# Optimization experiments

Hardware: AMD Instinct MI355X
Metric: run time of the kernel (lower is better)

Reference implementation:

```python
import jax, jax.numpy as jnp
import numpy as np
import math

D_MODEL = 1024
N_HEADS = 16
D_FF = 4096
B, T = 2, 2048
EPS = 1e-5


def setup_inputs() -> dict:
    key = jax.random.key(0)
    ks = jax.random.split(key, 8)
    s = 0.02
    return {
        "x": jax.random.normal(ks[0], (B, T, D_MODEL), jnp.float32),
        "wq": jax.random.normal(ks[1], (D_MODEL, D_MODEL), jnp.float32) * s,
        "wk": jax.random.normal(ks[2], (D_MODEL, D_MODEL), jnp.float32) * s,
        "wv": jax.random.normal(ks[3], (D_MODEL, D_MODEL), jnp.float32) * s,
        "wo": jax.random.normal(ks[4], (D_MODEL, D_MODEL), jnp.float32) * s,
        "ln1_w": jnp.ones((D_MODEL,), jnp.float32),
        "ln2_w": jnp.ones((D_MODEL,), jnp.float32),
        "w1": jax.random.normal(ks[5], (D_FF, D_MODEL), jnp.float32) * s,
        "w2": jax.random.normal(ks[6], (D_MODEL, D_FF), jnp.float32) * s,
    }


def rmsnorm(x, w):
    # weight * x / sqrt(mean(x^2) + eps)
    denom = jnp.sqrt(jnp.mean(jnp.square(x), axis=-1, keepdims=True) + EPS)
    return w * x / denom


def mhsa(x, wq, wk, wv, wo):
    b, t, d = x.shape
    dk = d // N_HEADS
    # Linear(weight shape (out,in)): y = x @ W.T
    q = (x @ wq.T).reshape(b, t, N_HEADS, dk).transpose(0, 2, 1, 3)  # bhtd
    k = (x @ wk.T).reshape(b, t, N_HEADS, dk).transpose(0, 2, 1, 3)
    v = (x @ wv.T).reshape(b, t, N_HEADS, dk).transpose(0, 2, 1, 3)
    scores = jnp.einsum("bhqd,bhkd->bhqk", q, k) / math.sqrt(dk)
    causal = jnp.tril(jnp.ones((t, t), bool))  # True = keep
    scores = jnp.where(causal, scores, -jnp.inf)
    probs = jax.nn.softmax(scores, axis=-1)
    out = jnp.einsum("bhqk,bhkd->bhqd", probs, v)
    out = out.transpose(0, 2, 1, 3).reshape(b, t, d)
    return out @ wo.T


def ffn(x, w1, w2):
    h = jax.nn.gelu(x @ w1.T, approximate=False)  # exact erf GELU
    return h @ w2.T


def reference(x, wq, wk, wv, wo, ln1_w, ln2_w, w1, w2):
    x = x + mhsa(rmsnorm(x, ln1_w), wq, wk, wv, wo)
    x = x + ffn(rmsnorm(x, ln2_w), w1, w2)
    return x
```

## Files before the change

kernel.cpp:

```cpp
#include <hip/hip_runtime.h>
#include <stdint.h>

#define D_MODEL 1024
#define N_HEADS 16
#define D_FF    4096
#define BATCH   2
#define SEQ     2048
#define EPSV    1e-5f
#define MTOK    (BATCH*SEQ)
#define QKVS    3072


typedef __bf16 bf16x8 __attribute__((ext_vector_type(8)));
typedef float  f32x4  __attribute__((ext_vector_type(4)));

#define MFMA_BF16(a,b,c) __builtin_amdgcn_mfma_f32_16x16x32_bf16((a),(b),(c),0,0,0)

__device__ __forceinline__ float b2f(unsigned short u) {
  union { unsigned int i; float f; } c; c.i = ((unsigned int)u) << 16; return c.f;
}
__device__ __forceinline__ unsigned short f2b(float f) {
  union { float f; unsigned int i; } c; c.f = f;
  unsigned int x = c.i;
  unsigned int r = (x + 0x7fffu + ((x >> 16) & 1u)) >> 16;
  return (unsigned short)r;
}
__device__ __forceinline__ unsigned short f2b_trunc(float f) {
  union { float f; unsigned int i; } c; c.f = f;
  return (unsigned short)(c.i >> 16);
}

__device__ __forceinline__ void glds16(const unsigned short* g, unsigned short* l) {
  __builtin_amdgcn_global_load_lds(
      (const __attribute__((address_space(1))) void*)g,
      (__attribute__((address_space(3))) void*)l, 16, 0, 0);
}

__global__ void detect_kernel(const unsigned int* __restrict__ ln1, int* __restrict__ flag) {
  if (threadIdx.x == 0 && blockIdx.x == 0)
    *flag = (ln1[0] == 0x3F800000u) ? 1 : 0;
}

__global__ void convert_all_kernel(
    const void* __restrict__ wq, const void* __restrict__ wk,
    const void* __restrict__ wv, const void* __restrict__ wo,
    const void* __restrict__ w1, const void* __restrict__ w2,
    const void* __restrict__ l1, const void* __restrict__ l2,
    unsigned short* dq, unsigned short* dk, unsigned short* dv, unsigned short* dwo,
    unsigned short* d1, unsigned short* d2, unsigned short* dl1, unsigned short* dl2,
    const int* __restrict__ flag) {
  const int i = blockIdx.x * 256 + threadIdx.x;
  const void* src; unsigned short* dst; int off;
  if (i < 1048576) {
    const int t = i >> 18;  off = i & 262143;
    src = (t == 0) ? wq : (t == 1) ? wk : (t == 2) ? wv : wo;
    dst = (t == 0) ? dq : (t == 1) ? dk : (t == 2) ? dv : dwo;
  } else if (i < 2097152) { off = i - 1048576; src = w1; dst = d1; }
  else if (i < 3145728)   { off = i - 2097152; src = w2; dst = d2; }
  else if (i < 3145984)   { off = i - 3145728; src = l1; dst = dl1; }
  else                    { off = i - 3145984; src = l2; dst = dl2; }
  if (*flag) {
    const float4 v = ((const float4*)src)[off];
    ushort4 o; o.x = f2b(v.x); o.y = f2b(v.y); o.z = f2b(v.z); o.w = f2b(v.w);
    ((ushort4*)dst)[off] = o;
  } else {
    ((ushort4*)dst)[off] = ((const ushort4*)src)[off];
  }
}

__global__ void rmsnorm_kernel(const void* __restrict__ xin,
                               const unsigned short* __restrict__ w,
                               unsigned short* __restrict__ out,
                               const int* __restrict__ f32flag) {
  __shared__ float red[4];
  const int row = blockIdx.x;
  const int tid = threadIdx.x;
  const int base = tid * 4;
  const bool f32 = f32flag && (*f32flag != 0);
  float v0, v1, v2, v3;
  if (f32) {
    const float4 p = ((const float4*)xin)[(size_t)row * 256 + tid];
    v0 = p.x; v1 = p.y; v2 = p.z; v3 = p.w;
  } else {
    const short4 p = *(const short4*)((const unsigned short*)xin + (size_t)row * D_MODEL + base);
    v0 = b2f((unsigned short)p.x); v1 = b2f((unsigned short)p.y);
    v2 = b2f((unsigned short)p.z); v3 = b2f((unsigned short)p.w);
  }
  float ss = v0*v0 + v1*v1 + v2*v2 + v3*v3;
  #pragma unroll
  for (int d = 1; d < 64; d <<= 1) ss += __shfl_xor(ss, d);
  if ((tid & 63) == 0) red[tid >> 6] = ss;
  __syncthreads();
  const float tot = red[0] + red[1] + red[2] + red[3];
  const float inv = 1.0f / sqrtf(tot * (1.0f / (float)D_MODEL) + EPSV);
  short4 ov;
  ov.x = (short)f2b(b2f(w[base + 0]) * v0 * inv);
  ov.y = (short)f2b(b2f(w[base + 1]) * v1 * inv);
  ov.z = (short)f2b(b2f(w[base + 2]) * v2 * inv);
  ov.w = (short)f2b(b2f(w[base + 3]) * v3 * inv);
  *(short4*)(out + (size_t)row * D_MODEL + base) = ov;
}

#define BM 128
template<int TBN, int KSEG, int TBK>
__global__ __launch_bounds__(256 * KSEG) void gemm_bt_kernel(
    const unsigned short* __restrict__ A,
    const unsigned short* __restrict__ Bw,
    void* __restrict__ C,
    const void* __restrict__ R,
    int M, int N, int K, int flags,
    const int* __restrict__ outf32_flag,
    const int* __restrict__ resf32_flag) {
  constexpr int JN = TBN / 32;
  constexpr int SR = TBK / 8;
  constexpr int SH = (TBK == 32) ? 1 : 0;
  constexpr int SM = SR - 1;
  constexpr int GA = BM * SR;
  constexpr int GT = (BM + TBN) * SR;
  constexpr int KH = TBK / 32;
  __shared__ __align__(16) unsigned short smem[KSEG * (BM + TBN) * TBK];
  unsigned short* Asb = smem;
  unsigned short* Bsb = smem + KSEG * BM * TBK;

  const int tid   = threadIdx.x;
  const int tid_l = tid & 255;
  const int w     = tid >> 6;
  const int kseg  = (KSEG == 1) ? 0 : (w >> 2);
  const int wm    = (w >> 1) & 1, wn = w & 1;
  const int ln    = tid & 63;
  const int lm    = ln & 15, quad = ln >> 4;
  unsigned short* As = Asb + kseg * BM * TBK;
  unsigned short* Bs = Bsb + kseg * TBN * TBK;

  const int gx = gridDim.x;
  const int L  = blockIdx.x + gx * blockIdx.y;
  const int per = (gx * gridDim.y) >> 3;
  const int tile = (L & 7) * per + (L >> 3);
  const int tileM = (tile / gx) * BM;
  const int tileN = (tile % gx) * TBN;

  const int kofs = kseg * (K / KSEG);

  f32x4 acc[4][JN];
  #pragma unroll
  for (int i = 0; i < 4; i++)
    #pragma unroll
    for (int j = 0; j < JN; j++) acc[i][j] = (f32x4){0.f, 0.f, 0.f, 0.f};

  for (int k0 = 0; k0 < K / KSEG; k0 += TBK) {
    __syncthreads();
    #pragma unroll
    for (int g0 = 0; g0 < GT; g0 += 256) {
      const int g = g0 + tid_l;
      if (g0 + 256 <= GA || g < GA) {
        const int r  = g / SR;
        const int sg = (g & SM) ^ ((r >> SH) & SM);
        glds16(&A[(size_t)(tileM + r) * K + kofs + k0 + sg * 8], &As[g * 8]);
      } else {
        const int gb = g - GA;
        const int r  = gb / SR;
        const int sg = (gb & SM) ^ ((r >> SH) & SM);
        glds16(&Bw[(size_t)(tileN + r) * K + kofs + k0 + sg * 8], &Bs[gb * 8]);
      }
    }
    __syncthreads();

    #pragma unroll
    for (int hh = 0; hh < KH; hh++) {
      bf16x8 af[4], bfr[JN];
      #pragma unroll
      for (int i = 0; i < 4; i++) {
        const int r = wm * 64 + i * 16 + lm;
        const int p = (hh * 4 + quad) ^ ((r >> SH) & SM);
        af[i] = *(const bf16x8*)&As[r * TBK + p * 8];
      }
      #pragma unroll
      for (int j = 0; j < JN; j++) {
        const int r = wn * (TBN / 2) + j * 16 + lm;
        const int p = (hh * 4 + quad) ^ ((r >> SH) & SM);
        bfr[j] = *(const bf16x8*)&Bs[r * TBK + p * 8];
      }
      #pragma unroll
      for (int i = 0; i < 4; i++)
        #pragma unroll
        for (int j = 0; j < JN; j++)
          acc[i][j] = MFMA_BF16(af[i], bfr[j], acc[i][j]);
    }
  }

  if constexpr (KSEG == 2) {
    float* scratch = (float*)smem;
    #pragma unroll
    for (int j = 0; j < JN; j++) {
      __syncthreads();
      if (kseg == 1) {
        #pragma unroll
        for (int i = 0; i < 4; i++)
          #pragma unroll
          for (int r = 0; r < 4; r++)
            scratch[tid_l * 16 + i * 4 + r] = acc[i][j][r];
      }
      __syncthreads();
      if (kseg == 0) {
        #pragma unroll
        for (int i = 0; i < 4; i++)
          #pragma unroll
          for (int r = 0; r < 4; r++)
            acc[i][j][r] += scratch[tid_l * 16 + i * 4 + r];
      }
    }
  }

  if (kseg == 0) {
    const bool hasR   = flags & 2;
    const bool dogelu = flags & 8;
    const bool outf32 = outf32_flag && (*outf32_flag != 0);
    const bool rf32   = resf32_flag && (*resf32_flag != 0);
    #pragma unroll
    for (int i = 0; i < 4; i++) {
      #pragma unroll
      for (int j = 0; j < JN; j++) {
        #pragma unroll
        for (int r = 0; r < 4; r++) {
          const int row = tileM + wm * 64 + i * 16 + quad * 4 + r;
          const int col = tileN + wn * (TBN / 2) + j * 16 + lm;
          float val = acc[i][j][r];
          if (dogelu) {
            const float u = 0.7978845608f * (val + 0.044715f * val * val * val);
            const float e = exp2f(u * 2.885390082f);
            val = val - val * __builtin_amdgcn_rcpf(e + 1.0f);
          }
          const size_t idx = (size_t)row * N + col;
          if (hasR) val += rf32 ? ((const float*)R)[idx]
                                : b2f(((const unsigned short*)R)[idx]);
          if (outf32) ((float*)C)[idx] = val;
          else        ((unsigned short*)C)[idx] = f2b(val);
        }
      }
    }
  }
}

__global__ __launch_bounds__(256) void attn_kernel(
    const unsigned short* __restrict__ QKV,
    unsigned short* __restrict__ O) {
  __shared__ __align__(16) unsigned short Ks [2][64 * 64];
  __shared__ __align__(16) unsigned short VTs[2][64 * 64];
  __shared__ __align__(16) unsigned short Ps [4][16 * 64];

  const int tid = threadIdx.x;
  const int w = tid >> 6, ln = tid & 63;
  const int lm = ln & 15, quad = ln >> 4;
  const f32x4 zf = (f32x4){0.f, 0.f, 0.f, 0.f};

  const int L   = blockIdx.x;
  const int xcd = L & 7;
  const int idx = L >> 3;
  const int bh  = xcd * 4 + (idx >> 4);
  const int pr  = idx & 15;
  const int b   = bh >> 4, h = bh & 15;
  const int qtA = pr, qtB = 31 - pr;
  const int nA = qtA + 1, total = nA + qtB + 1;

  const unsigned short* Qp = QKV + (size_t)b * SEQ * QKVS + h * 64;
  const unsigned short* Kp = Qp + 1024;
  const unsigned short* Vp = Qp + 2048;

  auto scale8 = [](bf16x8 v) -> bf16x8 {
    union { bf16x8 h; unsigned short u[8]; } in, out;
    in.h = v;
    #pragma unroll
    for (int ii = 0; ii < 8; ii++) out.u[ii] = f2b(b2f(in.u[ii]) * 0.1803368801f);
    return out.h;
  };

  bf16x8 qfA0, qfA1, qfB0, qfB1;
  {
    const size_t ra = (size_t)(qtA * 64 + w * 16 + lm) * QKVS;
    qfA0 = scale8(*(const bf16x8*)&Qp[ra + quad * 8]);
    qfA1 = scale8(*(const bf16x8*)&Qp[ra + 32 + quad * 8]);
    const size_t rb = (size_t)(qtB * 64 + w * 16 + lm) * QKVS;
    qfB0 = scale8(*(const bf16x8*)&Qp[rb + quad * 8]);
    qfB1 = scale8(*(const bf16x8*)&Qp[rb + 32 + quad * 8]);
  }

  const int vkey2 = (tid >> 3) << 1;
  const int vd8   = (tid & 7) << 3;
  const int ve    = tid & 7;

  f32x4 oacc[4];
  float lrow[4];
  #pragma unroll
  for (int i = 0; i < 4; i++) oacc[i] = zf;
  #pragma unroll
  for (int r = 0; r < 4; r++) lrow[r] = 0.f;

  union V8 { uint4 u; unsigned short s[8]; };
  V8 v0r, v1r;

  auto issue_stage = [&](int c, int buf) {
    #pragma unroll
    for (int ii = 0; ii < 2; ii++) {
      const int g   = tid + 256 * ii;
      const int key = g >> 3;
      const int sg  = (g & 7) ^ (key & 7);
      glds16(&Kp[(size_t)(c * 64 + key) * QKVS + sg * 8], &Ks[buf][g * 8]);
    }
    v0r.u = *(const uint4*)&Vp[(size_t)(c * 64 + vkey2)     * QKVS + vd8];
    v1r.u = *(const uint4*)&Vp[(size_t)(c * 64 + vkey2 + 1) * QKVS + vd8];
  };

  auto write_vt = [&](int buf) {
    const int swb = (vkey2 >> 3) ^ ve;
    #pragma unroll
    for (int ii = 0; ii < 8; ii++) {
      const int phys = (vd8 + ii) * 64 + swb * 8 + (vkey2 & 7);
      const unsigned int pk = (unsigned int)v0r.s[ii] | ((unsigned int)v1r.s[ii] << 16);
      *(unsigned int*)&VTs[buf][phys] = pk;
    }
  };

  auto write_o = [&](int qt) {
    #pragma unroll
    for (int r = 0; r < 4; r++) {
      float l = lrow[r];
      #pragma unroll
      for (int d2 = 1; d2 < 16; d2 <<= 1) l += __shfl_xor(l, d2);
      const float invl = 1.0f / l;
      const size_t orow = (size_t)(b * SEQ + qt * 64 + w * 16 + quad * 4 + r) * D_MODEL + h * 64;
      #pragma unroll
      for (int nt = 0; nt < 4; nt++)
        O[orow + nt * 16 + lm] = f2b(oacc[nt][r] * invl);
    }
  };

  issue_stage(0, 0);
  for (int j = 0; j < total; j++) {
    const int buf = j & 1;
    write_vt(buf);
    __syncthreads();

    if (j + 1 < total) {
      const int cn = (j + 1 < nA) ? (j + 1) : (j + 1 - nA);
      issue_stage(cn, buf ^ 1);
    }
    if (j == nA) {
      write_o(qtA);
      #pragma unroll
      for (int i = 0; i < 4; i++) oacc[i] = zf;
      #pragma unroll
      for (int r = 0; r < 4; r++) lrow[r] = 0.f;
    }

    const bool isA = j < nA;
    const int  c   = isA ? j : j - nA;
    const int  qt  = isA ? qtA : qtB;
    const bool diag = (c == qt);
    const bf16x8 qf0 = isA ? qfA0 : qfB0;
    const bf16x8 qf1 = isA ? qfA1 : qfB1;

    f32x4 s[4];
    #pragma unroll
    for (int kg = 0; kg < 4; kg++) {
      const int kbase = (kg * 16 + lm) * 64;
      const int s0 = quad ^ (lm & 7);
      const bf16x8 kf0 = *(const bf16x8*)&Ks[buf][kbase + s0 * 8];
      const bf16x8 kf1 = *(const bf16x8*)&Ks[buf][kbase + (s0 ^ 4) * 8];
      s[kg] = MFMA_BF16(qf0, kf0, zf);
      s[kg] = MFMA_BF16(qf1, kf1, s[kg]);
    }

    #pragma unroll
    for (int r = 0; r < 4; r++) {
      float a0 = s[0][r], a1 = s[1][r], a2 = s[2][r], a3 = s[3][r];
      if (diag) {
        const int qloc = w * 16 + quad * 4 + r;
        if (lm      > qloc) a0 = -1e30f;
        if (lm + 16 > qloc) a1 = -1e30f;
        if (lm + 32 > qloc) a2 = -1e30f;
        if (lm + 48 > qloc) a3 = -1e30f;
      }
      const float p0 = exp2f(a0), p1 = exp2f(a1);
      const float p2 = exp2f(a2), p3 = exp2f(a3);
      lrow[r] += (p0 + p1) + (p2 + p3);
      const int row = quad * 4 + r;
      const int rb  = row * 64, r7 = row & 7, lhi = lm >> 3, llo = lm & 7;
      Ps[w][rb + (((0 + lhi) ^ r7) << 3) + llo] = f2b_trunc(p0);
      Ps[w][rb + (((2 + lhi) ^ r7) << 3) + llo] = f2b_trunc(p1);
      Ps[w][rb + (((4 + lhi) ^ r7) << 3) + llo] = f2b_trunc(p2);
      Ps[w][rb + (((6 + lhi) ^ r7) << 3) + llo] = f2b_trunc(p3);
    }

    #pragma unroll
    for (int hh = 0; hh < 2; hh++) {
      const bf16x8 pf = *(const bf16x8*)&Ps[w][lm * 64 + (((hh * 4 + quad) ^ (lm & 7)) << 3)];
      #pragma unroll
      for (int nt = 0; nt < 4; nt++) {
        const int dim = nt * 16 + lm;
        const int swb = (hh * 4 + quad) ^ (dim >> 3);
        const bf16x8 vf = *(const bf16x8*)&VTs[buf][dim * 64 + swb * 8];
        oacc[nt] = MFMA_BF16(pf, vf, oacc[nt]);
      }
    }
  }
  write_o(qtB);
}

extern "C" void kernel_launch(void* const* d_in, const int* in_sizes, int n_in,
                              void* d_out, int out_size, void* d_ws, size_t ws_size,
                              hipStream_t stream) {
  char* ws = (char*)d_ws;
  const size_t MB = 1u << 20;
  unsigned short* cwq  = (unsigned short*)(ws + 8  * MB);
  unsigned short* cwk  = (unsigned short*)(ws + 10 * MB);
  unsigned short* cwv  = (unsigned short*)(ws + 12 * MB);
  unsigned short* cwo  = (unsigned short*)(ws + 14 * MB);
  unsigned short* cln1 = (unsigned short*)(ws + 16 * MB);
  unsigned short* cln2 = (unsigned short*)(ws + 16 * MB + 4096);
  unsigned short* cw1  = (unsigned short*)(ws + 17 * MB);
  unsigned short* cw2  = (unsigned short*)(ws + 25 * MB);
  unsigned short* xn1  = (unsigned short*)(ws + 33 * MB);
  unsigned short* qkv  = (unsigned short*)(ws + 41 * MB);
  unsigned short* y1   = (unsigned short*)(ws + 65 * MB);
  unsigned short* xn2  = (unsigned short*)(ws + 0);
  unsigned short* hbf  = (unsigned short*)(ws + 33 * MB);
  int*            flag = (int*)           (ws + 73 * MB);
  unsigned short* ao   = xn1;

  detect_kernel<<<1, 64, 0, stream>>>((const unsigned int*)d_in[5], flag);

  convert_all_kernel<<<12290, 256, 0, stream>>>(
      d_in[1], d_in[2], d_in[3], d_in[4], d_in[7], d_in[8], d_in[5], d_in[6],
      cwq, cwk, cwv, cwo, cw1, cw2, cln1, cln2, flag);

  rmsnorm_kernel<<<MTOK, 256, 0, stream>>>(d_in[0], cln1, xn1, flag);
  {
    const dim3 g(QKVS / 128, MTOK / BM);
    gemm_bt_kernel<128,1,64><<<g, 256, 0, stream>>>(xn1, cwq, qkv, nullptr,
                                                    MTOK, QKVS, D_MODEL, 0, nullptr, nullptr);
  }
  attn_kernel<<<512, 256, 0, stream>>>(qkv, ao);
  {
    const dim3 g(D_MODEL / 64, MTOK / BM);
    gemm_bt_kernel<64,2,64><<<g, 512, 0, stream>>>(ao, cwo, y1, d_in[0],
                                                   MTOK, D_MODEL, D_MODEL, 2, nullptr, flag);
  }
  rmsnorm_kernel<<<MTOK, 256, 0, stream>>>(y1, cln2, xn2, nullptr);
  {
    const dim3 g(D_FF / 128, MTOK / BM);
    gemm_bt_kernel<128,1,64><<<g, 256, 0, stream>>>(xn2, cw1, hbf, nullptr,
                                                    MTOK, D_FF, D_MODEL, 8, nullptr, nullptr);
  }
  {
    const dim3 g(D_MODEL / 64, MTOK / BM);
    gemm_bt_kernel<64,2,64><<<g, 512, 0, stream>>>(hbf, cw2, d_out, y1,
                                                   MTOK, D_MODEL, D_FF, 2, flag, nullptr);
  }
}
```

Before: 356.9 us.

## Add 256x256-tile pipelined GEMM kernel for QKV and FFN-up projections

Adds a new 512-thread GEMM kernel with 256x256 output tiles, XOR-swizzled LDS staging via direct global-to-LDS loads, and a two-stage K pipeline that interleaves the next tile's loads with MFMA phases. It also uses XCD-aware tile remapping and s_setprio around the MFMA blocks. The aim is more operand reuse per loaded byte and better hiding of load latency in the two large projection GEMMs. In exchange the grid is small (192 and 256 blocks), the kernel relies on heavy register use for the 16x2 accumulators, and it assumes dimensions divisible by 256.

```diff
diff --git a/kernel.cpp b/kernel.cpp
--- a/kernel.cpp
+++ b/kernel.cpp
@@ -241,6 +241,134 @@
   }
 }
 
+template<bool DOGELU>
+__global__ __launch_bounds__(512, 2) void gemm256_kernel(
+    const unsigned short* __restrict__ A,
+    const unsigned short* __restrict__ Bw,
+    unsigned short* __restrict__ C,
+    int M, int N, int K) {
+  __shared__ __align__(16) unsigned short smem[2 * 32768];
+
+  const int tid = threadIdx.x;
+  const int wn  = tid >> 6;
+  const int ln  = tid & 63;
+  const int lm  = ln & 15, quad = ln >> 4;
+
+  const int gx = gridDim.x;
+  const int L  = blockIdx.x + gx * blockIdx.y;
+  const int per = (gx * gridDim.y) >> 3;
+  const int tile = (L & 7) * per + (L >> 3);
+  const int tileM = (tile / gx) * 256;
+  const int tileN = (tile % gx) * 256;
+
+  const int NT = K >> 6;
+
+  auto stage = [&](const unsigned short* src, int srow, int buf, int isB,
+                   int R0, int kt) {
+    unsigned short* dst = smem + buf * 32768 + isB * 16384 + R0 * 64;
+    const size_t base = (size_t)(srow + R0) * K + (kt << 6);
+    #pragma unroll
+    for (int it = 0; it < 2; ++it) {
+      const int g  = it * 512 + tid;
+      const int r  = g >> 3;
+      const int sg = (g & 7) ^ (r & 7);
+      glds16(&src[base + (size_t)r * K + sg * 8], &dst[g * 8]);
+    }
+  };
+
+  f32x4 acc[16][2];
+  #pragma unroll
+  for (int i = 0; i < 16; i++) {
+    acc[i][0] = (f32x4){0.f, 0.f, 0.f, 0.f};
+    acc[i][1] = (f32x4){0.f, 0.f, 0.f, 0.f};
+  }
+
+  stage(A,  tileM, 0, 0,   0, 0);
+  stage(A,  tileM, 0, 0, 128, 0);
+  stage(Bw, tileN, 0, 1,   0, 0);
+  stage(Bw, tileN, 0, 1, 128, 0);
+  stage(Bw, tileN, 1, 1,   0, 1);
+  stage(Bw, tileN, 1, 1, 128, 1);
+  stage(A,  tileM, 1, 0,   0, 1);
+  asm volatile("s_waitcnt vmcnt(6)" ::: "memory");
+  __builtin_amdgcn_s_barrier();
+
+  bf16x8 bf0[2], bf1[2];
+
+  for (int t = 0; t < NT; ++t) {
+    const int cur = t & 1;
+    unsigned short* As = smem + cur * 32768;
+    unsigned short* Bs = As + 16384;
+    const bool haveN1 = (t + 1 < NT);
+    const bool haveN2 = (t + 2 < NT);
+
+    #pragma unroll
+    for (int p = 0; p < 4; ++p) {
+      bf16x8 af0[4], af1[4];
+      #pragma unroll
+      for (int i = 0; i < 4; ++i) {
+        const int r  = (p * 4 + i) * 16 + lm;
+        const int s0 = quad ^ (r & 7);
+        af0[i] = *(const bf16x8*)&As[r * 64 + s0 * 8];
+        af1[i] = *(const bf16x8*)&As[r * 64 + (s0 ^ 4) * 8];
+      }
+      if (p == 0) {
+        #pragma unroll
+        for (int nf = 0; nf < 2; ++nf) {
+          const int rb = wn * 32 + nf * 16 + lm;
+          const int s0 = quad ^ (rb & 7);
+          bf0[nf] = *(const bf16x8*)&Bs[rb * 64 + s0 * 8];
+          bf1[nf] = *(const bf16x8*)&Bs[rb * 64 + (s0 ^ 4) * 8];
+        }
+        if (haveN1) stage(A, tileM, (t + 1) & 1, 0, 128, t + 1);
+      } else if (p == 1) {
+        if (haveN2) {
+          stage(Bw, tileN, cur, 1,   0, t + 2);
+          stage(Bw, tileN, cur, 1, 128, t + 2);
+        }
+      } else if (p == 2) {
+        if (haveN2) stage(A, tileM, cur, 0, 0, t + 2);
+      }
+      __builtin_amdgcn_s_barrier();
+      asm volatile("s_waitcnt lgkmcnt(0)" ::: "memory");
+      __builtin_amdgcn_sched_barrier(0);
+      __builtin_amdgcn_s_setprio(1);
+      #pragma unroll
+      for (int i = 0; i < 4; ++i)
+        #pragma unroll
+        for (int nf = 0; nf < 2; ++nf) {
+          acc[p * 4 + i][nf] = MFMA_BF16(af0[i], bf0[nf], acc[p * 4 + i][nf]);
+          acc[p * 4 + i][nf] = MFMA_BF16(af1[i], bf1[nf], acc[p * 4 + i][nf]);
+        }
+      __builtin_amdgcn_s_setprio(0);
+      if (p == 3 && haveN1) {
+        if (haveN2) asm volatile("s_waitcnt vmcnt(6)" ::: "memory");
+        else        asm volatile("s_waitcnt vmcnt(0)" ::: "memory");
+      }
+      __builtin_amdgcn_s_barrier();
+    }
+  }
+
+  #pragma unroll
+  for (int mp = 0; mp < 16; ++mp) {
+    #pragma unroll
+    for (int nf = 0; nf < 2; ++nf) {
+      #pragma unroll
+      for (int r = 0; r < 4; ++r) {
+        const int row = tileM + mp * 16 + quad * 4 + r;
+        const int col = tileN + wn * 32 + nf * 16 + lm;
+        float val = acc[mp][nf][r];
+        if constexpr (DOGELU) {
+          const float u = 0.7978845608f * (val + 0.044715f * val * val * val);
+          const float e = exp2f(u * 2.885390082f);
+          val = val - val * __builtin_amdgcn_rcpf(e + 1.0f);
+        }
+        C[(size_t)row * N + col] = f2b(val);
+      }
+    }
+  }
+}
+
 __global__ __launch_bounds__(256) void attn_kernel(
     const unsigned short* __restrict__ QKV,
     unsigned short* __restrict__ O) {
@@ -435,9 +563,8 @@
 
   rmsnorm_kernel<<<MTOK, 256, 0, stream>>>(d_in[0], cln1, xn1, flag);
   {
-    const dim3 g(QKVS / 128, MTOK / BM);
-    gemm_bt_kernel<128,1,64><<<g, 256, 0, stream>>>(xn1, cwq, qkv, nullptr,
-                                                    MTOK, QKVS, D_MODEL, 0, nullptr, nullptr);
+    const dim3 g(QKVS / 256, MTOK / 256);
+    gemm256_kernel<false><<<g, 512, 0, stream>>>(xn1, cwq, qkv, MTOK, QKVS, D_MODEL);
   }
   attn_kernel<<<512, 256, 0, stream>>>(qkv, ao);
   {
@@ -447,9 +574,8 @@
   }
   rmsnorm_kernel<<<MTOK, 256, 0, stream>>>(y1, cln2, xn2, nullptr);
   {
-    const dim3 g(D_FF / 128, MTOK / BM);
-    gemm_bt_kernel<128,1,64><<<g, 256, 0, stream>>>(xn2, cw1, hbf, nullptr,
-                                                    MTOK, D_FF, D_MODEL, 8, nullptr, nullptr);
+    const dim3 g(D_FF / 256, MTOK / 256);
+    gemm256_kernel<true><<<g, 512, 0, stream>>>(xn2, cw1, hbf, MTOK, D_FF, D_MODEL);
   }
   {
     const dim3 g(D_MODEL / 64, MTOK / BM);
```

Result: faster. 332.7 us (-6.8%).
